# Kernel tuning notes

Hardware: AMD Instinct MI355X
Metric: run time of the kernel (lower is better)

Reference implementation:

```python
import jax, jax.numpy as jnp
import numpy as np

# --- hashgrid config (from __init__: num_levels=16, level_dim=4, base_res=2, log2_hashmap_size=19, desired_res=2048) ---
NUM_LEVELS = 16
LEVEL_DIM = 4
BASE_RES = 2
DESIRED_RES = 2048
TABLE_SIZE = 2 ** 19
_b = np.exp((np.log(DESIRED_RES) - np.log(BASE_RES)) / (NUM_LEVELS - 1))
SCALES = BASE_RES * _b ** np.arange(NUM_LEVELS) - 1.0          # instant-ngp per-level scale
RES = (np.ceil(SCALES) + 1).astype(np.int64)                   # per-level grid resolution
PRIME = np.uint32(2654435761)                                  # 2D spatial hash prime


def softplus10(x):
    return jax.nn.softplus(10.0 * x) / 10.0


def hash_encode(u, tables):
    """u: [P,2] in [0,1]; tables: [L, TABLE_SIZE, LEVEL_DIM]. Returns [P, L*LEVEL_DIM]."""
    outs = []
    for l in range(NUM_LEVELS):
        s = float(SCALES[l])
        res = int(RES[l])
        pos = u * s + 0.5
        pf = jnp.floor(pos)
        fr = pos - pf                      # bilinear fractions, [P,2]
        pi = pf.astype(jnp.int32)
        acc = None
        for dx in (0, 1):
            for dy in (0, 1):
                cx = pi[:, 0] + dx
                cy = pi[:, 1] + dy
                if res * res <= TABLE_SIZE:
                    idx = cy * res + cx                                   # dense level
                else:
                    idx = (cx.astype(jnp.uint32) ^ (cy.astype(jnp.uint32) * PRIME)) % jnp.uint32(TABLE_SIZE)
                    idx = idx.astype(jnp.int32)                           # hashed level
                wx = fr[:, 0] if dx else 1.0 - fr[:, 0]
                wy = fr[:, 1] if dy else 1.0 - fr[:, 1]
                term = tables[l][idx] * (wx * wy)[:, None]                # gather + bilerp
                acc = term if acc is None else acc + term
        outs.append(acc)
    return jnp.concatenate(outs, axis=-1)


def setup_inputs() -> dict:
    key = jax.random.key(0)
    ks = jax.random.split(key, 4)
    B, N, T = 4, 2048, 192
    x = jax.random.normal(ks[0], (B, N, T, 2), jnp.float32)
    embeddings = jax.random.normal(ks[1], (NUM_LEVELS, TABLE_SIZE, LEVEL_DIM), jnp.float32) * 1e-2
    W0 = jax.random.normal(ks[2], (64, 64), jnp.float32) / 8.0
    b0 = jnp.zeros((64,), jnp.float32)
    W1 = jax.random.normal(ks[3], (64, 1), jnp.float32) / 8.0
    b1 = jnp.zeros((1,), jnp.float32)
    return {"x": x, "embeddings": embeddings, "W0": W0, "b0": b0, "W1": W1, "b1": b1}


def reference(x, embeddings, W0, b0, W1, b1):
    B, N, T = x.shape[:3]
    xf = x.reshape(-1, T, 2)                       # [B*N, T, 2]
    rays_o = xf[:, 0]
    rd = xf[:, -1] - xf[:, 0]
    rd = rd / jnp.linalg.norm(rd, axis=-1, keepdims=True)
    z = jnp.linspace(0.0, 2.0, T)                  # [T]
    sample_dist = 1.0 / T
    xys = rays_o[:, None, :] + rd[:, None, :] * z[None, :, None]   # [B*N, T, 2]
    xys = jnp.clip(xys, -1.0, 1.0)                 # aabb clamp [-1,-1,1,1]
    u = (xys.reshape(-1, 2) + 1.0) * 0.5           # map [-bound,bound] -> [0,1], bound=1
    feats = hash_encode(u, embeddings)             # [P, 64]
    h = softplus10(feats @ W0 + b0)
    sigma = softplus10(h @ W1 + b1).reshape(-1, T) # [B*N, T]
    deltas = jnp.concatenate([jnp.full((1,), sample_dist, sigma.dtype), z[1:] - z[:-1]])  # [T]
    density = (deltas[None, :] * sigma).reshape(B, N, T)
    return density
```

## Files before the change

kernel.cpp:

```cpp
#include <hip/hip_runtime.h>
#include <cmath>

#define NUM_LEVELS 16
#define TABLE_SIZE 524288
#define TMASK (TABLE_SIZE - 1)
#define HASH_PRIME 2654435761u
#define T_SAMPLES 192
#define BLOCK 256
#define PTS 64

typedef __bf16 bf16x8 __attribute__((ext_vector_type(8)));
typedef __bf16 bf16x4 __attribute__((ext_vector_type(4)));
typedef float f32x4 __attribute__((ext_vector_type(4)));

struct LvlParams {
    float s[NUM_LEVELS];
    int   res[NUM_LEVELS];
    int   hashed[NUM_LEVELS];
};

__device__ __forceinline__ float softplus10(float x) {
    float t = 10.0f * x;
    float e = __expf(-fabsf(t));
    return (fmaxf(t, 0.0f) + __logf(1.0f + e)) * 0.1f;
}

__device__ __forceinline__ void corner_idx(int cx, int cy, int res, int hashed,
                                           int& i00, int& i01, int& i10, int& i11) {
    if (hashed) {
        unsigned hy0 = (unsigned)cy * HASH_PRIME;
        unsigned hy1 = (unsigned)(cy + 1) * HASH_PRIME;
        i00 = (int)(((unsigned)cx ^ hy0) & TMASK);
        i01 = (int)(((unsigned)cx ^ hy1) & TMASK);
        i10 = (int)(((unsigned)(cx + 1) ^ hy0) & TMASK);
        i11 = (int)(((unsigned)(cx + 1) ^ hy1) & TMASK);
    } else {
        i00 = cy * res + cx; i10 = i00 + 1;
        i01 = i00 + res;     i11 = i01 + 1;
    }
}

__device__ __forceinline__ bf16x4 lerp4(f32x4 c00, f32x4 c01, f32x4 c10, f32x4 c11,
                                        float fx, float fy) {
    float w00 = (1.0f - fx) * (1.0f - fy), w01 = (1.0f - fx) * fy;
    float w10 = fx * (1.0f - fy),          w11 = fx * fy;
    f32x4 a = c00 * w00 + c01 * w01 + c10 * w10 + c11 * w11;
    bf16x4 r;
    r[0] = (__bf16)a.x; r[1] = (__bf16)a.y; r[2] = (__bf16)a.z; r[3] = (__bf16)a.w;
    return r;
}

__global__ void prep(const float* __restrict__ W0, __bf16* __restrict__ w0f,
                     float* __restrict__ sArr, int* __restrict__ resArr,
                     int* __restrict__ hashArr, LvlParams lp) {
    const int t = threadIdx.x;
    if (t < NUM_LEVELS) {
        sArr[t] = lp.s[t]; resArr[t] = lp.res[t]; hashArr[t] = lp.hashed[t];
    }
    #pragma unroll
    for (int i = 0; i < 16; ++i) {
        int f = t * 16 + i;
        int j = f & 7, lx = (f >> 3) & 15, q = (f >> 7) & 3, nt = (f >> 9) & 3, kc = f >> 11;
        int k = kc * 32 + q * 8 + j;
        int n = nt * 16 + lx;
        w0f[f] = (__bf16)W0[k * 64 + n];
    }
}

__launch_bounds__(BLOCK, 8)
__global__ void nerf_fused(const float* __restrict__ x,
                           const float* __restrict__ emb,
                           const __bf16* __restrict__ w0f,
                           const float* __restrict__ sArr,
                           const int* __restrict__ resArr,
                           const int* __restrict__ hashArr,
                           const float* __restrict__ b0,
                           const float* __restrict__ W1,
                           const float* __restrict__ b1,
                           float* __restrict__ out) {
    __shared__ __align__(16) __bf16 feT[NUM_LEVELS * PTS * 4];

    const int tid  = threadIdx.x;
    const int lane = tid & 63, w = tid >> 6;

    const int gp  = blockIdx.x * PTS + lane;
    const int ray = gp / T_SAMPLES;
    const int t   = gp - ray * T_SAMPLES;

    const float2 o  = *(const float2*)(x + (size_t)ray * (T_SAMPLES * 2));
    const float2 ep = *(const float2*)(x + (size_t)ray * (T_SAMPLES * 2) + (T_SAMPLES - 1) * 2);
    float rdx = ep.x - o.x, rdy = ep.y - o.y;
    float inv = 1.0f / sqrtf(rdx * rdx + rdy * rdy);
    rdx *= inv; rdy *= inv;
    const float z = (float)((double)t * (2.0 / 191.0));
    float px = fminf(fmaxf(o.x + rdx * z, -1.0f), 1.0f);
    float py = fminf(fmaxf(o.y + rdy * z, -1.0f), 1.0f);
    const float ux = (px + 1.0f) * 0.5f;
    const float uy = (py + 1.0f) * 0.5f;

    const int l0 = w, l1 = w + 4, l2 = w + 8, l3 = w + 12;

    f32x4 c3v[4]; float fx3, fy3;
    {
        float s = sArr[l3];
        float posx = ux * s + 0.5f, posy = uy * s + 0.5f;
        float pfx = floorf(posx), pfy = floorf(posy);
        fx3 = posx - pfx; fy3 = posy - pfy;
        int cx = (int)pfx, cy = (int)pfy;
        int i00, i01, i10, i11;
        corner_idx(cx, cy, resArr[l3], hashArr[l3], i00, i01, i10, i11);
        const f32x4* tb = (const f32x4*)(emb + (size_t)l3 * (TABLE_SIZE * 4));
        c3v[0] = tb[i00]; c3v[1] = tb[i01]; c3v[2] = tb[i10]; c3v[3] = tb[i11];
    }

    {
        float s = sArr[l2];
        float posx = ux * s + 0.5f, posy = uy * s + 0.5f;
        float pfx = floorf(posx), pfy = floorf(posy);
        float fx = posx - pfx, fy = posy - pfy;
        int cx = (int)pfx, cy = (int)pfy;
        int res = resArr[l2];
        int i00 = cy * res + cx, i10 = i00 + 1, i01 = i00 + res, i11 = i01 + 1;
        const f32x4* tb = (const f32x4*)(emb + (size_t)l2 * (TABLE_SIZE * 4));
        f32x4 a = tb[i00], b = tb[i01], c = tb[i10], d = tb[i11];
        *(bf16x4*)&feT[(l2 * PTS + lane) * 4] = lerp4(a, b, c, d, fx, fy);
    }

    {
        float s = sArr[l1];
        float posx = ux * s + 0.5f, posy = uy * s + 0.5f;
        float pfx = floorf(posx), pfy = floorf(posy);
        float fx = posx - pfx, fy = posy - pfy;
        int cx = (int)pfx, cy = (int)pfy;
        int res = resArr[l1];
        int i00 = cy * res + cx, i10 = i00 + 1, i01 = i00 + res, i11 = i01 + 1;
        const f32x4* tb = (const f32x4*)(emb + (size_t)l1 * (TABLE_SIZE * 4));
        f32x4 a = tb[i00], b = tb[i01], c = tb[i10], d = tb[i11];
        *(bf16x4*)&feT[(l1 * PTS + lane) * 4] = lerp4(a, b, c, d, fx, fy);
    }

    {
        float s = sArr[l0];
        float posx = ux * s + 0.5f, posy = uy * s + 0.5f;
        float pfx = floorf(posx), pfy = floorf(posy);
        float fx = posx - pfx, fy = posy - pfy;
        int cx = (int)pfx, cy = (int)pfy;
        int res = resArr[l0];
        int i00 = cy * res + cx, i10 = i00 + 1, i01 = i00 + res, i11 = i01 + 1;
        const f32x4* tb = (const f32x4*)(emb + (size_t)l0 * (TABLE_SIZE * 4));
        f32x4 a = tb[i00], b = tb[i01], c = tb[i10], d = tb[i11];
        *(bf16x4*)&feT[(l0 * PTS + lane) * 4] = lerp4(a, b, c, d, fx, fy);
    }

    *(bf16x4*)&feT[(l3 * PTS + lane) * 4] = lerp4(c3v[0], c3v[1], c3v[2], c3v[3], fx3, fy3);

    __syncthreads();

    const int lx = lane & 15, q = lane >> 4;
    const int p  = w * 16 + lx;

    f32x4 acc[4];
    #pragma unroll
    for (int nt = 0; nt < 4; ++nt) acc[nt] = (f32x4)(0.0f);

    #pragma unroll
    for (int kc = 0; kc < 2; ++kc) {
        const int la = kc * 8 + 2 * q;
        bf16x4 lo = *(const bf16x4*)&feT[(la * PTS + p) * 4];
        bf16x4 hi = *(const bf16x4*)&feT[((la + 1) * PTS + p) * 4];
        bf16x8 afr = __builtin_shufflevector(lo, hi, 0, 1, 2, 3, 4, 5, 6, 7);
        #pragma unroll
        for (int nt = 0; nt < 4; ++nt) {
            bf16x8 bfr = *(const bf16x8*)(w0f + (size_t)(((kc * 4 + nt) * 4 + q) * 16 + lx) * 8);
            acc[nt] = __builtin_amdgcn_mfma_f32_16x16x32_bf16(afr, bfr, acc[nt], 0, 0, 0);
        }
    }

    float b0v[4], w1v[4];
    #pragma unroll
    for (int nt = 0; nt < 4; ++nt) {
        b0v[nt] = b0[nt * 16 + lx];
        w1v[nt] = W1[nt * 16 + lx];
    }
    const float b1v = b1[0];
    const float d0 = (float)(1.0 / 192.0);
    const float d1 = (float)(2.0 / 191.0);

    float part[4];
    #pragma unroll
    for (int r = 0; r < 4; ++r) {
        float pp = 0.0f;
        #pragma unroll
        for (int nt = 0; nt < 4; ++nt)
            pp += softplus10(acc[nt][r] + b0v[nt]) * w1v[nt];
        pp += __shfl_xor(pp, 1, 64);
        pp += __shfl_xor(pp, 2, 64);
        pp += __shfl_xor(pp, 4, 64);
        pp += __shfl_xor(pp, 8, 64);
        part[r] = pp;
    }
    if (lx == 0) {
        const int g0 = blockIdx.x * PTS + w * 16 + q * 4;
        const int tt = g0 % T_SAMPLES;
        f32x4 ov;
        ov.x = softplus10(part[0] + b1v) * (tt == 0 ? d0 : d1);
        ov.y = softplus10(part[1] + b1v) * d1;
        ov.z = softplus10(part[2] + b1v) * d1;
        ov.w = softplus10(part[3] + b1v) * d1;
        *(f32x4*)(out + g0) = ov;
    }
}

extern "C" void kernel_launch(void* const* d_in, const int* in_sizes, int n_in,
                              void* d_out, int out_size, void* d_ws, size_t ws_size,
                              hipStream_t stream) {
    const float* x   = (const float*)d_in[0];
    const float* emb = (const float*)d_in[1];
    const float* W0  = (const float*)d_in[2];
    const float* b0  = (const float*)d_in[3];
    const float* W1  = (const float*)d_in[4];
    const float* b1  = (const float*)d_in[5];
    float* out = (float*)d_out;

    char* ws = (char*)d_ws;
    __bf16* w0f   = (__bf16*)ws;
    float* sArr   = (float*)(ws + 8192);
    int*   resArr = (int*)(ws + 8256);
    int*   hashArr= (int*)(ws + 8320);

    LvlParams lp;
    const double bb = std::exp((std::log(2048.0) - std::log(2.0)) / 15.0);
    for (int l = 0; l < NUM_LEVELS; ++l) {
        double sc = 2.0 * std::pow(bb, (double)l) - 1.0;
        int rr = (int)std::ceil(sc) + 1;
        lp.s[l] = (float)sc;
        lp.res[l] = rr;
        lp.hashed[l] = ((long long)rr * (long long)rr > (long long)TABLE_SIZE) ? 1 : 0;
    }

    prep<<<1, 256, 0, stream>>>(W0, w0f, sArr, resArr, hashArr, lp);

    const int nblk = out_size / PTS;
    nerf_fused<<<nblk, BLOCK, 0, stream>>>(x, emb, w0f, sArr, resArr, hashArr,
                                           b0, W1, b1, out);
}
```

Baseline: 378.7 us.

## Quantize embedding tables to int16 with per-chunk scales before gathering

Adds a per-call prepass that converts the used part of each level's fp32 embedding table into int16 with one absmax scale per 4096-entry chunk, packed into a compact workspace buffer. The fused kernel then gathers 8-byte int16 corners instead of 16-byte fp32 corners and dequantizes with the chunk scale. The aim is to halve gather traffic and cache footprint for the random hash lookups. In exchange it adds a full read of the hashed tables every call, extra scale loads, and quantization error. It falls back to the fp32 path when the workspace is too small.

```diff
diff --git a/kernel.cpp b/kernel.cpp
--- a/kernel.cpp
+++ b/kernel.cpp
@@ -1,5 +1,6 @@
 #include <hip/hip_runtime.h>
 #include <cmath>
+#include <algorithm>
 
 #define NUM_LEVELS 16
 #define TABLE_SIZE 524288
@@ -8,15 +9,19 @@
 #define T_SAMPLES 192
 #define BLOCK 256
 #define PTS 64
+#define CHUNK 4096
 
 typedef __bf16 bf16x8 __attribute__((ext_vector_type(8)));
 typedef __bf16 bf16x4 __attribute__((ext_vector_type(4)));
 typedef float f32x4 __attribute__((ext_vector_type(4)));
+typedef short s16x4 __attribute__((ext_vector_type(4)));
 
 struct LvlParams {
     float s[NUM_LEVELS];
     int   res[NUM_LEVELS];
     int   hashed[NUM_LEVELS];
+    int   off[NUM_LEVELS];
+    int   used[NUM_LEVELS];
 };
 
 __device__ __forceinline__ float softplus10(float x) {
@@ -52,10 +57,12 @@
 
 __global__ void prep(const float* __restrict__ W0, __bf16* __restrict__ w0f,
                      float* __restrict__ sArr, int* __restrict__ resArr,
-                     int* __restrict__ hashArr, LvlParams lp) {
+                     int* __restrict__ hashArr, int* __restrict__ offArr,
+                     int* __restrict__ usedArr, LvlParams lp) {
     const int t = threadIdx.x;
     if (t < NUM_LEVELS) {
         sArr[t] = lp.s[t]; resArr[t] = lp.res[t]; hashArr[t] = lp.hashed[t];
+        offArr[t] = lp.off[t]; usedArr[t] = lp.used[t];
     }
     #pragma unroll
     for (int i = 0; i < 16; ++i) {
@@ -67,13 +74,65 @@
     }
 }
 
+__global__ void prep_tables(const float* __restrict__ emb, short* __restrict__ embq,
+                            float* __restrict__ scaleArr,
+                            const int* __restrict__ offArr, const int* __restrict__ usedArr) {
+    __shared__ float red[256];
+    const int l    = blockIdx.y;
+    const int used = usedArr[l];
+    const int base = blockIdx.x * CHUNK;
+    if (base >= used) return;
+    const int t = threadIdx.x;
+    const float* src = emb + ((size_t)l * TABLE_SIZE + base) * 4;
+
+    f32x4 v[16];
+    float m = 0.0f;
+    #pragma unroll
+    for (int i = 0; i < 16; ++i) {
+        int e = t + 256 * i;
+        if (base + e < used) {
+            v[i] = *(const f32x4*)(src + (size_t)e * 4);
+            m = fmaxf(m, fmaxf(fmaxf(fabsf(v[i].x), fabsf(v[i].y)),
+                               fmaxf(fabsf(v[i].z), fabsf(v[i].w))));
+        } else v[i] = (f32x4)(0.0f);
+    }
+    red[t] = m;
+    __syncthreads();
+    for (int s = 128; s > 0; s >>= 1) {
+        if (t < s) red[t] = fmaxf(red[t], red[t + s]);
+        __syncthreads();
+    }
+    const float mx  = red[0];
+    const float inv = (mx > 0.0f) ? (32767.0f / mx) : 0.0f;
+    const int chunkIdx = (offArr[l] >> 12) + blockIdx.x;
+    if (t == 0) scaleArr[chunkIdx] = (mx > 0.0f) ? (mx / 32767.0f) : 0.0f;
+
+    short* dst = embq + (size_t)(offArr[l] + base) * 4;
+    #pragma unroll
+    for (int i = 0; i < 16; ++i) {
+        int e = t + 256 * i;
+        if (base + e < used) {
+            s16x4 q;
+            q[0] = (short)__float2int_rn(v[i].x * inv);
+            q[1] = (short)__float2int_rn(v[i].y * inv);
+            q[2] = (short)__float2int_rn(v[i].z * inv);
+            q[3] = (short)__float2int_rn(v[i].w * inv);
+            *(s16x4*)(dst + (size_t)e * 4) = q;
+        }
+    }
+}
+
+template<bool QT>
 __launch_bounds__(BLOCK, 8)
 __global__ void nerf_fused(const float* __restrict__ x,
                            const float* __restrict__ emb,
+                           const short* __restrict__ embq,
+                           const float* __restrict__ scaleArr,
                            const __bf16* __restrict__ w0f,
                            const float* __restrict__ sArr,
                            const int* __restrict__ resArr,
                            const int* __restrict__ hashArr,
+                           const int* __restrict__ offArr,
                            const float* __restrict__ b0,
                            const float* __restrict__ W1,
                            const float* __restrict__ b1,
@@ -98,7 +157,7 @@
     const float ux = (px + 1.0f) * 0.5f;
     const float uy = (py + 1.0f) * 0.5f;
 
-    const int l0 = w, l1 = w + 4, l2 = w + 8, l3 = w + 12;
+    const int l3 = w + 12;
 
     f32x4 c3v[4]; float fx3, fy3;
     {
@@ -109,47 +168,44 @@
         int cx = (int)pfx, cy = (int)pfy;
         int i00, i01, i10, i11;
         corner_idx(cx, cy, resArr[l3], hashArr[l3], i00, i01, i10, i11);
-        const f32x4* tb = (const f32x4*)(emb + (size_t)l3 * (TABLE_SIZE * 4));
-        c3v[0] = tb[i00]; c3v[1] = tb[i01]; c3v[2] = tb[i10]; c3v[3] = tb[i11];
-    }
-
-    {
-        float s = sArr[l2];
+        if (QT) {
+            const s16x4* tb = (const s16x4*)embq + offArr[l3];
+            const int cb = offArr[l3] >> 12;
+            s16x4 r0 = tb[i00], r1 = tb[i01], r2 = tb[i10], r3 = tb[i11];
+            c3v[0] = __builtin_convertvector(r0, f32x4) * scaleArr[cb + (i00 >> 12)];
+            c3v[1] = __builtin_convertvector(r1, f32x4) * scaleArr[cb + (i01 >> 12)];
+            c3v[2] = __builtin_convertvector(r2, f32x4) * scaleArr[cb + (i10 >> 12)];
+            c3v[3] = __builtin_convertvector(r3, f32x4) * scaleArr[cb + (i11 >> 12)];
+        } else {
+            const f32x4* tb = (const f32x4*)(emb + (size_t)l3 * (TABLE_SIZE * 4));
+            c3v[0] = tb[i00]; c3v[1] = tb[i01]; c3v[2] = tb[i10]; c3v[3] = tb[i11];
+        }
+    }
+
+    #pragma unroll
+    for (int li = 0; li < 3; ++li) {
+        const int l = w + li * 4;
+        float s = sArr[l];
         float posx = ux * s + 0.5f, posy = uy * s + 0.5f;
         float pfx = floorf(posx), pfy = floorf(posy);
         float fx = posx - pfx, fy = posy - pfy;
         int cx = (int)pfx, cy = (int)pfy;
-        int res = resArr[l2];
+        int res = resArr[l];
         int i00 = cy * res + cx, i10 = i00 + 1, i01 = i00 + res, i11 = i01 + 1;
-        const f32x4* tb = (const f32x4*)(emb + (size_t)l2 * (TABLE_SIZE * 4));
-        f32x4 a = tb[i00], b = tb[i01], c = tb[i10], d = tb[i11];
-        *(bf16x4*)&feT[(l2 * PTS + lane) * 4] = lerp4(a, b, c, d, fx, fy);
-    }
-
-    {
-        float s = sArr[l1];
-        float posx = ux * s + 0.5f, posy = uy * s + 0.5f;
-        float pfx = floorf(posx), pfy = floorf(posy);
-        float fx = posx - pfx, fy = posy - pfy;
-        int cx = (int)pfx, cy = (int)pfy;
-        int res = resArr[l1];
-        int i00 = cy * res + cx, i10 = i00 + 1, i01 = i00 + res, i11 = i01 + 1;
-        const f32x4* tb = (const f32x4*)(emb + (size_t)l1 * (TABLE_SIZE * 4));
-        f32x4 a = tb[i00], b = tb[i01], c = tb[i10], d = tb[i11];
-        *(bf16x4*)&feT[(l1 * PTS + lane) * 4] = lerp4(a, b, c, d, fx, fy);
-    }
-
-    {
-        float s = sArr[l0];
-        float posx = ux * s + 0.5f, posy = uy * s + 0.5f;
-        float pfx = floorf(posx), pfy = floorf(posy);
-        float fx = posx - pfx, fy = posy - pfy;
-        int cx = (int)pfx, cy = (int)pfy;
-        int res = resArr[l0];
-        int i00 = cy * res + cx, i10 = i00 + 1, i01 = i00 + res, i11 = i01 + 1;
-        const f32x4* tb = (const f32x4*)(emb + (size_t)l0 * (TABLE_SIZE * 4));
-        f32x4 a = tb[i00], b = tb[i01], c = tb[i10], d = tb[i11];
-        *(bf16x4*)&feT[(l0 * PTS + lane) * 4] = lerp4(a, b, c, d, fx, fy);
+        f32x4 a, b, c, d;
+        if (QT) {
+            const s16x4* tb = (const s16x4*)embq + offArr[l];
+            const int cb = offArr[l] >> 12;
+            s16x4 r0 = tb[i00], r1 = tb[i01], r2 = tb[i10], r3 = tb[i11];
+            a = __builtin_convertvector(r0, f32x4) * scaleArr[cb + (i00 >> 12)];
+            b = __builtin_convertvector(r1, f32x4) * scaleArr[cb + (i01 >> 12)];
+            c = __builtin_convertvector(r2, f32x4) * scaleArr[cb + (i10 >> 12)];
+            d = __builtin_convertvector(r3, f32x4) * scaleArr[cb + (i11 >> 12)];
+        } else {
+            const f32x4* tb = (const f32x4*)(emb + (size_t)l * (TABLE_SIZE * 4));
+            a = tb[i00]; b = tb[i01]; c = tb[i10]; d = tb[i11];
+        }
+        *(bf16x4*)&feT[(l * PTS + lane) * 4] = lerp4(a, b, c, d, fx, fy);
     }
 
     *(bf16x4*)&feT[(l3 * PTS + lane) * 4] = lerp4(c3v[0], c3v[1], c3v[2], c3v[3], fx3, fy3);
@@ -223,24 +279,52 @@
     float* out = (float*)d_out;
 
     char* ws = (char*)d_ws;
-    __bf16* w0f   = (__bf16*)ws;
-    float* sArr   = (float*)(ws + 8192);
-    int*   resArr = (int*)(ws + 8256);
-    int*   hashArr= (int*)(ws + 8320);
+    __bf16* w0f    = (__bf16*)ws;
+    float*  sArr   = (float*)(ws + 8192);
+    int*    resArr = (int*)(ws + 8256);
+    int*    hashArr= (int*)(ws + 8320);
+    int*    offArr = (int*)(ws + 8384);
+    int*    usedArr= (int*)(ws + 8448);
+    float*  scaleArr = (float*)(ws + 8704);
+    short*  embq   = (short*)(ws + 16384);
 
     LvlParams lp;
     const double bb = std::exp((std::log(2048.0) - std::log(2.0)) / 15.0);
+    int off = 0, maxUsed = 0;
     for (int l = 0; l < NUM_LEVELS; ++l) {
         double sc = 2.0 * std::pow(bb, (double)l) - 1.0;
         int rr = (int)std::ceil(sc) + 1;
         lp.s[l] = (float)sc;
         lp.res[l] = rr;
         lp.hashed[l] = ((long long)rr * (long long)rr > (long long)TABLE_SIZE) ? 1 : 0;
-    }
-
-    prep<<<1, 256, 0, stream>>>(W0, w0f, sArr, resArr, hashArr, lp);
+        int used;
+        if (lp.hashed[l]) {
+            used = TABLE_SIZE;
+        } else {
+            long long cmax = (long long)std::floor(sc + 0.5) + 1;
+            long long u = cmax * (long long)rr + cmax + 1 + (rr + 2);
+            used = (int)std::min((long long)TABLE_SIZE, u);
+        }
+        lp.off[l]  = off;
+        lp.used[l] = used;
+        off += (used + CHUNK - 1) & ~(CHUNK - 1);
+        if (used > maxUsed) maxUsed = used;
+    }
+    const size_t need = 16384 + (size_t)off * 4 * sizeof(short);
+    const bool useQ = ws_size >= need;
+
+    prep<<<1, 256, 0, stream>>>(W0, w0f, sArr, resArr, hashArr, offArr, usedArr, lp);
 
     const int nblk = out_size / PTS;
-    nerf_fused<<<nblk, BLOCK, 0, stream>>>(x, emb, w0f, sArr, resArr, hashArr,
-                                           b0, W1, b1, out);
-}
+    if (useQ) {
+        dim3 pg((maxUsed + CHUNK - 1) / CHUNK, NUM_LEVELS);
+        prep_tables<<<pg, 256, 0, stream>>>(emb, embq, scaleArr, offArr, usedArr);
+        nerf_fused<true><<<nblk, BLOCK, 0, stream>>>(x, emb, embq, scaleArr, w0f,
+                                                     sArr, resArr, hashArr, offArr,
+                                                     b0, W1, b1, out);
+    } else {
+        nerf_fused<false><<<nblk, BLOCK, 0, stream>>>(x, emb, embq, scaleArr, w0f,
+                                                      sArr, resArr, hashArr, offArr,
+                                                      b0, W1, b1, out);
+    }
+}
```

Measured after the change: 355.6 us. 6.1% less time.
